# Kernel optimization log

Measured on AMD Instinct MI355X. Metric: run time of the kernel, lower is better.

Reference implementation:

```python
import jax, jax.numpy as jnp
import numpy as np

T, B, C, HF, H, W, E, TOP_K = 4, 32, 384, 1536, 14, 14, 8, 2
AUX_W = 0.01
ALPHA = 2.0  # spikingjelly ATan surrogate default

@jax.custom_vjp
def spike(v):
    return (v >= 0.0).astype(v.dtype)

def _spike_fwd(v):
    return spike(v), v

def _spike_bwd(v, g):
    sg = (ALPHA / 2.0) / (1.0 + (jnp.pi / 2.0 * ALPHA * v) ** 2)
    return (g * sg,)

spike.defvjp(_spike_fwd, _spike_bwd)

def lif_multistep(x, tau):
    # x: (T, ...). decay_input=True, v_threshold=1, hard reset to 0, detach_reset
    def step(v, xt):
        v = v + (xt - v) / tau
        s = spike(v - 1.0)
        v = v * (1.0 - jax.lax.stop_gradient(s))
        return v, s
    _, s = jax.lax.scan(step, jnp.zeros_like(x[0]), x)
    return s

def bn_eval(y, gamma, beta, mean, var, eps=1e-5):
    inv = gamma / jnp.sqrt(var + eps)
    return y * inv[None, :, None, None] + (beta - mean * inv)[None, :, None, None]

def setup_inputs() -> dict:
    key = jax.random.key(0)
    ks = jax.random.split(key, 8)
    d = {"x": jax.random.normal(ks[0], (T, B, C, H, W), jnp.float32)}
    d["rw"] = jax.random.normal(ks[1], (E, C), jnp.float32) * 0.02
    d["rb"] = jnp.zeros((E,), jnp.float32)
    d["r_gamma"] = jnp.ones((E,), jnp.float32)
    d["r_beta"] = jnp.zeros((E,), jnp.float32)
    d["r_mean"] = jax.random.normal(ks[2], (E,), jnp.float32) * 0.01
    d["r_var"] = jax.random.uniform(ks[3], (E,), jnp.float32, 0.75, 1.25)
    d["w1"] = jax.random.normal(ks[4], (E, HF, C), jnp.float32) * 0.02
    d["b1"] = jnp.zeros((E, HF), jnp.float32)
    d["g1"] = jnp.ones((E, HF), jnp.float32)
    d["be1"] = jnp.zeros((E, HF), jnp.float32)
    d["m1"] = jax.random.normal(ks[5], (E, HF), jnp.float32) * 0.01
    d["v1"] = jnp.ones((E, HF), jnp.float32)
    d["w2"] = jax.random.normal(ks[6], (E, C, HF), jnp.float32) * 0.02
    d["b2"] = jnp.zeros((E, C), jnp.float32)
    d["g2"] = jnp.ones((E, C), jnp.float32)
    d["be2"] = jnp.zeros((E, C), jnp.float32)
    d["m2"] = jax.random.normal(ks[7], (E, C), jnp.float32) * 0.01
    d["v2"] = jnp.ones((E, C), jnp.float32)
    d["taus"] = jnp.linspace(1.5, 4.0, E, dtype=jnp.float32)
    return d

def reference(x, rw, rb, r_gamma, r_beta, r_mean, r_var,
              w1, b1, g1, be1, m1, v1, w2, b2, g2, be2, m2, v2, taus):
    Tn, Bn, Cn, Hn, Wn = x.shape
    N = Tn * Bn
    # ---- SpikeRouter ----
    s = lif_multistep(x, 2.0)                                   # (T,B,C,H,W)
    r = jnp.einsum('tbchw,ec->tbehw', s, rw) + rb[None, None, :, None, None]
    r = bn_eval(r.reshape(N, E, Hn, Wn), r_gamma, r_beta, r_mean, r_var)
    logits = r.mean(axis=(-2, -1))                              # (N,E)
    probs = jax.nn.softmax(logits, axis=-1)
    tkw, tki = jax.lax.top_k(probs, TOP_K)
    tkw = tkw / tkw.sum(axis=-1, keepdims=True)
    one_hot = jax.nn.one_hot(tki, E, dtype=x.dtype)             # (N,K,E)
    gate = (one_hot * tkw[..., None]).sum(axis=1)               # (N,E), 0 for unselected
    # ---- expert dispatch/combine (dense, math-equivalent: gate==0 masks out) ----
    xt = x.reshape(N, Cn, Hn, Wn)
    out = jnp.zeros_like(xt)
    for e in range(E):
        s1 = spike(xt / taus[e] - 1.0)                          # T=1 LIF step
        h = jnp.einsum('nchw,oc->nohw', s1, w1[e]) + b1[e][None, :, None, None]
        h = bn_eval(h, g1[e], be1[e], m1[e], v1[e])
        s2 = spike(h / taus[e] - 1.0)
        o = jnp.einsum('nchw,oc->nohw', s2, w2[e]) + b2[e][None, :, None, None]
        o = bn_eval(o, g2[e], be2[e], m2[e], v2[e])
        o = o + xt                                              # final residual
        out = out + gate[:, e, None, None, None] * o
    # ---- Switch-style load balancing loss ----
    f = one_hot.sum(axis=1).mean(axis=0)                        # fraction routed per expert
    p = probs.mean(axis=0)
    aux = AUX_W * E * jnp.sum(f * p)
    return out.reshape(Tn, Bn, Cn, Hn, Wn), aux
```

## Files before the change

kernel.cpp:

```cpp
#include <hip/hip_runtime.h>
#include <hip/hip_bf16.h>
#include <cstdint>
#include <math.h>

#define T_  4
#define B_  32
#define C_  384
#define HF_ 1536
#define HW_ 196
#define E_  8
#define N_  128
#define NROW 1792
#define NGT  50176
#define LCAP 64

#define LIFW (B_ * C_ / 4)
#define TRB  (E_ * 12 * 24)
#define PRB  48
#define COMBB ((N_ * C_ * 49) / 256)

__global__ __launch_bounds__(256) void k_lifprep(
    const float* __restrict__ x, float* __restrict__ cnt,
    unsigned int* __restrict__ levels4,
    const float* __restrict__ w1, __hip_bfloat16* __restrict__ w1t,
    const float* b1, const float* g1, const float* be1,
    const float* m1, const float* v1,
    const float* b2, const float* g2, const float* be2,
    const float* m2, const float* v2,
    const float* taus,
    float* A, float* Bc, float* const2, float* inv2v,
    float* rowmaxp, int* header) {
  __shared__ float tile[64][33];
  int blk = blockIdx.x;
  int tid = threadIdx.x;

  if (blk < LIFW) {
    int lane = tid & 63, wave = tid >> 6;
    int bc = blk * 4 + wave;
    bool act = lane < 49;
    float te[E_];
    #pragma unroll
    for (int e2 = 0; e2 < E_; ++e2) {
      float t = taus[e2];
      float y = t;
      #pragma unroll
      for (int it = 0; it < 4; ++it) {
        float cnd = __uint_as_float(__float_as_uint(y) - 1u);
        if (cnd / t - 1.0f >= 0.0f) y = cnd; else break;
      }
      te[e2] = y;
    }
    const float4* xr = (const float4*)x;
    size_t rb = (size_t)bc * 49 + (act ? lane : 0);
    const size_t ts4 = (size_t)B_ * C_ * 49;
    float4 v = {0.f, 0.f, 0.f, 0.f};
    unsigned int counts = 0;
    unsigned int pk[T_];
    #pragma unroll
    for (int t = 0; t < T_; ++t) {
      float4 xv;
      if (act) xv = xr[rb + (size_t)t * ts4];
      else { xv.x = xv.y = xv.z = xv.w = -1e30f; }
      int l0 = 0, l1 = 0, l2 = 0, l3 = 0;
      #pragma unroll
      for (int e2 = 0; e2 < E_; ++e2) {
        l0 += (xv.x >= te[e2]) ? 1 : 0;
        l1 += (xv.y >= te[e2]) ? 1 : 0;
        l2 += (xv.z >= te[e2]) ? 1 : 0;
        l3 += (xv.w >= te[e2]) ? 1 : 0;
      }
      pk[t] = (unsigned int)l0 | ((unsigned int)l1 << 8) |
              ((unsigned int)l2 << 16) | ((unsigned int)l3 << 24);
      v.x = v.x + (xv.x - v.x) * 0.5f;
      v.y = v.y + (xv.y - v.y) * 0.5f;
      v.z = v.z + (xv.z - v.z) * 0.5f;
      v.w = v.w + (xv.w - v.w) * 0.5f;
      int cl = 0;
      if (v.x - 1.0f >= 0.0f) { v.x = 0.f; ++cl; }
      if (v.y - 1.0f >= 0.0f) { v.y = 0.f; ++cl; }
      if (v.z - 1.0f >= 0.0f) { v.z = 0.f; ++cl; }
      if (v.w - 1.0f >= 0.0f) { v.w = 0.f; ++cl; }
      counts += (unsigned int)cl << (8 * t);
    }
    if (act) {
      #pragma unroll
      for (int t = 0; t < T_; ++t)
        levels4[rb + (size_t)t * ts4] = pk[t];
    }
    #pragma unroll
    for (int off = 1; off < 64; off <<= 1)
      counts += (unsigned int)__shfl_xor((int)counts, off, 64);
    if (lane == 0) {
      #pragma unroll
      for (int t = 0; t < T_; ++t)
        cnt[(size_t)t * B_ * C_ + bc] = (float)((counts >> (8 * t)) & 0xffu);
    }
  } else if (blk < LIFW + TRB) {
    int rem = blk - LIFW;
    int e = rem / 288, r2 = rem % 288;
    int ct = r2 / 24, ot = r2 % 24;
    int c0 = ct * 32, o0 = ot * 64;
    int cl = tid & 31, olb = tid >> 5;
    #pragma unroll
    for (int it = 0; it < 8; ++it) {
      int ol = olb + it * 8;
      tile[ol][cl] = w1[(size_t)(e * HF_ + o0 + ol) * C_ + c0 + cl];
    }
    __syncthreads();
    int ol2 = tid & 63, clb = tid >> 6;
    #pragma unroll
    for (int it = 0; it < 8; ++it) {
      int cl2 = clb + it * 4;
      w1t[(size_t)(e * C_ + c0 + cl2) * HF_ + o0 + ol2] =
          __float2bfloat16(tile[ol2][cl2]);
    }
    if (tid < 32) {
      float m = 0.f;
      for (int ol = 0; ol < 64; ++ol) {
        float bv = __bfloat162float(__float2bfloat16(tile[ol][tid]));
        m = fmaxf(m, fabsf(bv));
      }
      rowmaxp[(size_t)(e * C_ + c0 + tid) * 24 + ot] = m;
    }
  } else {
    int idx = (blk - LIFW - TRB) * 256 + tid;
    if (idx < 64) header[idx] = 0;
    if (idx < E_ * HF_) {
      int e = idx / HF_;
      float inv = g1[idx] / sqrtf(v1[idx] + 1e-5f);
      float sh  = be1[idx] - m1[idx] * inv;
      A[idx]  = inv;
      Bc[idx] = inv * b1[idx] + sh - taus[e];
    }
    if (idx < E_ * C_) {
      float inv = g2[idx] / sqrtf(v2[idx] + 1e-5f);
      const2[idx] = b2[idx] * inv + (be2[idx] - m2[idx] * inv);
      inv2v[idx]  = inv;
    }
  }
}

__global__ __launch_bounds__(256) void k_router(
    const float* __restrict__ cnt, const float* __restrict__ rw,
    const float* rb, const float* rg, const float* rbeta,
    const float* rmean, const float* rvar,
    const float* __restrict__ const2,
    const float* __restrict__ rowmaxp, float* __restrict__ rowmax,
    const float* __restrict__ A, const float* __restrict__ Bc,
    float* __restrict__ thrmin,
    int* sel_e, float* sel_g, float* gsum, float* K,
    float* f_acc, float* p_acc) {
  __shared__ float sc[C_ + 256 + E_];
  __shared__ int s_i1, s_i2;
  __shared__ float s_g1, s_g2;
  int bid = blockIdx.x, tid = threadIdx.x;

  if (bid < N_) {
    int n = bid;
    float* part = sc + C_;
    float* lg = part + 256;
    for (int c = tid; c < C_; c += 256) sc[c] = cnt[(size_t)n * C_ + c];
    __syncthreads();
    {
      int e = tid >> 5, sub = tid & 31;
      float d = 0.f;
      for (int c = sub; c < C_; c += 32) d += rw[e * C_ + c] * sc[c];
      part[tid] = d;
    }
    __syncthreads();
    if (tid < E_) {
      float dot = 0.f;
      #pragma unroll
      for (int j = 0; j < 32; ++j) dot += part[tid * 32 + j];
      float inv = rg[tid] / sqrtf(rvar[tid] + 1e-5f);
      lg[tid] = (dot * (1.0f / HW_) + rb[tid]) * inv +
                (rbeta[tid] - rmean[tid] * inv);
    }
    __syncthreads();
    if (tid == 0) {
      float m = lg[0];
      for (int e = 1; e < E_; ++e) m = fmaxf(m, lg[e]);
      float pr[E_]; float s = 0.f;
      for (int e = 0; e < E_; ++e) { pr[e] = expf(lg[e] - m); s += pr[e]; }
      float invs = 1.0f / s;
      for (int e = 0; e < E_; ++e) pr[e] *= invs;
      int i1 = 0;
      for (int e = 1; e < E_; ++e) if (pr[e] > pr[i1]) i1 = e;
      int i2 = (i1 == 0) ? 1 : 0;
      for (int e = 0; e < E_; ++e) if (e != i1 && pr[e] > pr[i2]) i2 = e;
      float w = pr[i1] + pr[i2];
      float ga = pr[i1] / w, gb = pr[i2] / w;
      sel_e[2 * n] = i1; sel_e[2 * n + 1] = i2;
      sel_g[2 * n] = ga; sel_g[2 * n + 1] = gb;
      gsum[n] = ga + gb;
      s_i1 = i1; s_i2 = i2; s_g1 = ga; s_g2 = gb;
      atomicAdd(&f_acc[i1], 1.0f);
      atomicAdd(&f_acc[i2], 1.0f);
      for (int e = 0; e < E_; ++e) atomicAdd(&p_acc[e], pr[e]);
    }
    __syncthreads();
    int i1 = s_i1, i2 = s_i2; float ga = s_g1, gb = s_g2;
    for (int c = tid; c < C_; c += 256)
      K[(size_t)n * C_ + c] =
          ga * const2[i1 * C_ + c] + gb * const2[i2 * C_ + c];
  } else if (bid < N_ + 12) {
    int idx = (bid - N_) * 256 + tid;
    if (idx < E_ * C_) {
      float m = 0.f;
      #pragma unroll
      for (int t = 0; t < 24; ++t) m = fmaxf(m, rowmaxp[(size_t)idx * 24 + t]);
      rowmax[idx] = m;
    }
  } else {
    float* red = sc;
    for (int e = 0; e < E_; ++e) {
      float m = INFINITY;
      for (int o = tid; o < HF_; o += 256) {
        float a = A[e * HF_ + o], b = Bc[e * HF_ + o];
        float thr = (a != 0.0f) ? (-b / fabsf(a))
                                : ((b >= 0.0f) ? -INFINITY : INFINITY);
        m = fminf(m, thr);
      }
      red[tid] = m;
      __syncthreads();
      for (int s = 128; s > 0; s >>= 1) {
        if (tid < s) red[tid] = fminf(red[tid], red[tid + s]);
        __syncthreads();
      }
      if (tid == 0) thrmin[e] = red[0];
      __syncthreads();
    }
  }
}

__global__ __launch_bounds__(256) void k_lists(
    const float* __restrict__ x, const unsigned char* __restrict__ levels,
    const int* __restrict__ sel_e,
    const float* __restrict__ rowmax, const float* __restrict__ thrmin,
    unsigned short* __restrict__ list16,
    int* __restrict__ queue, int* __restrict__ qcount,
    const float* __restrict__ f_acc, const float* __restrict__ p_acc,
    float* __restrict__ aux_out,
    const float* __restrict__ gsum, const float* __restrict__ K,
    float* __restrict__ out) {
  __shared__ unsigned char xs8[14 * C_];
  int bid = blockIdx.x, tid = threadIdx.x;

  if (bid >= NROW) {
    int idx = (bid - NROW) * 256 + tid;
    int nc = idx / 49;
    float g = gsum[nc / C_];
    float kc = K[nc];
    float4 v = ((const float4*)x)[idx];
    v.x = g * v.x + kc;
    v.y = g * v.y + kc;
    v.z = g * v.z + kc;
    v.w = g * v.w + kc;
    ((float4*)out)[idx] = v;
    return;
  }

  int lane = tid & 63, wave = tid >> 6;
  int n = bid / 14, h = bid - n * 14;
  unsigned long long lmask = (1ull << lane) - 1ull;

  if (bid == 0 && tid == 0) {
    float s = 0.f;
    for (int e = 0; e < E_; ++e)
      s += (f_acc[e] * (1.0f / N_)) * (p_acc[e] * (1.0f / N_));
    *aux_out = 0.01f * E_ * s;
  }

  for (int c = tid; c < C_; c += 256) {
    const unsigned short* p =
        (const unsigned short*)(levels + (size_t)(n * C_ + c) * HW_ + h * 14);
    #pragma unroll
    for (int i = 0; i < 7; ++i) {
      unsigned short u = p[i];
      xs8[(2 * i) * C_ + c]     = (unsigned char)(u & 0xff);
      xs8[(2 * i + 1) * C_ + c] = (unsigned char)(u >> 8);
    }
  }
  __syncthreads();

  for (int t = wave; t < 28; t += 4) {
    int k = t / 14, w = t - k * 14;
    int pair = 2 * n + k;
    int e = sel_e[pair];
    const float* rme = rowmax + e * C_;
    unsigned long long masks[6];
    int nnz = 0;
    float myb = 0.f;
    #pragma unroll
    for (int cb = 0; cb < 6; ++cb) {
      int c = cb * 64 + lane;
      bool sp = ((int)xs8[w * C_ + c] > e);
      unsigned long long m = __ballot(sp);
      masks[cb] = m;
      if (sp) myb += rme[c];
      nnz += __popcll(m);
    }
    #pragma unroll
    for (int off = 1; off < 64; off <<= 1) myb += __shfl_xor(myb, off, 64);
    bool prune = (myb < thrmin[e] - 1e-4f);
    if (!prune) {
      int tw = pair * 196 + h * 14 + w;
      size_t lbase = (size_t)tw * LCAP;
      int cum = 0;
      #pragma unroll
      for (int cb = 0; cb < 6; ++cb) {
        unsigned long long m = masks[cb];
        bool sp = (m >> lane) & 1ull;
        int pos = cum + __popcll(m & lmask);
        if (sp && pos < LCAP) list16[lbase + pos] = (unsigned short)(cb * 64 + lane);
        cum += __popcll(m);
      }
      if (lane == 0) {
        int nv = nnz < LCAP ? nnz : LCAP;
        int qi = atomicAdd(qcount, 1);
        queue[qi] = tw | (nv << 20);
      }
    }
  }
}

__global__ __launch_bounds__(256, 4) void k_gather(
    const __hip_bfloat16* __restrict__ w1t,
    const float* __restrict__ A, const float* __restrict__ Bc,
    const int* __restrict__ sel_e, const float* __restrict__ sel_g,
    const int* __restrict__ queue, const int* __restrict__ qcount,
    const unsigned short* __restrict__ list16,
    const float* __restrict__ inv2v, const float* __restrict__ w2,
    float* __restrict__ out) {
  int nq = *qcount;
  int wid = blockIdx.x * 4 + (threadIdx.x >> 6);
  int lane = threadIdx.x & 63;
  int nwaves = gridDim.x * 4;

  for (int qi = wid; qi < nq; qi += nwaves) {
    int ent = queue[qi];
    int tw = ent & 0xFFFFF;
    int nnz = ent >> 20;
    int pair = tw / HW_, pos = tw - pair * HW_;
    int n = pair >> 1;
    int e = sel_e[pair];
    int lv = (int)list16[(size_t)tw * LCAP + lane];
    const uint4* wb = (const uint4*)(w1t + (size_t)e * C_ * HF_);

    #pragma unroll
    for (int pass = 0; pass < 3; ++pass) {
      const uint4* wbp = wb + pass * 64 + lane;
      float acc[8];
      #pragma unroll
      for (int q = 0; q < 8; ++q) acc[q] = 0.f;
      int j = 0;
      for (; j + 4 <= nnz; j += 4) {
        int c0 = __shfl(lv, j + 0);
        int c1 = __shfl(lv, j + 1);
        int c2 = __shfl(lv, j + 2);
        int c3 = __shfl(lv, j + 3);
        uint4 a = wbp[c0 * 192];
        uint4 b = wbp[c1 * 192];
        uint4 c = wbp[c2 * 192];
        uint4 d = wbp[c3 * 192];
        uint32_t ua[4] = {a.x, a.y, a.z, a.w};
        uint32_t ub[4] = {b.x, b.y, b.z, b.w};
        uint32_t uc[4] = {c.x, c.y, c.z, c.w};
        uint32_t ud[4] = {d.x, d.y, d.z, d.w};
        #pragma unroll
        for (int q = 0; q < 4; ++q) {
          acc[2 * q]     += __uint_as_float(ua[q] << 16) + __uint_as_float(ub[q] << 16) +
                            __uint_as_float(uc[q] << 16) + __uint_as_float(ud[q] << 16);
          acc[2 * q + 1] += __uint_as_float(ua[q] & 0xffff0000u) + __uint_as_float(ub[q] & 0xffff0000u) +
                            __uint_as_float(uc[q] & 0xffff0000u) + __uint_as_float(ud[q] & 0xffff0000u);
        }
      }
      for (; j < nnz; ++j) {
        int c0 = __shfl(lv, j);
        uint4 a = wbp[c0 * 192];
        uint32_t ua[4] = {a.x, a.y, a.z, a.w};
        #pragma unroll
        for (int q = 0; q < 4; ++q) {
          acc[2 * q]     += __uint_as_float(ua[q] << 16);
          acc[2 * q + 1] += __uint_as_float(ua[q] & 0xffff0000u);
        }
      }
      int k2 = (pass * 64 + lane) * 2;
      float4 Av0 = ((const float4*)(A + e * HF_))[k2];
      float4 Av1 = ((const float4*)(A + e * HF_))[k2 + 1];
      float4 Bv0 = ((const float4*)(Bc + e * HF_))[k2];
      float4 Bv1 = ((const float4*)(Bc + e * HF_))[k2 + 1];
      float av[8] = {Av0.x, Av0.y, Av0.z, Av0.w, Av1.x, Av1.y, Av1.z, Av1.w};
      float bv[8] = {Bv0.x, Bv0.y, Bv0.z, Bv0.w, Bv1.x, Bv1.y, Bv1.z, Bv1.w};
      #pragma unroll
      for (int q = 0; q < 8; ++q) {
        unsigned long long fm = __ballot(av[q] * acc[q] + bv[q] >= 0.0f);
        while (fm) {
          int b = __ffsll((unsigned long long)fm) - 1;
          fm &= fm - 1;
          int o = (pass * 64 + b) * 8 + q;
          float gk = sel_g[pair];
          const float* w2r = w2 + (size_t)e * C_ * HF_ + o;
          const float* ivr = inv2v + e * C_;
          for (int c = lane; c < C_; c += 64) {
            atomicAdd(&out[((size_t)(n * C_ + c)) * HW_ + pos],
                      gk * ivr[c] * w2r[(size_t)c * HF_]);
          }
        }
      }
    }
  }
}

extern "C" void kernel_launch(void* const* d_in, const int* in_sizes, int n_in,
                              void* d_out, int out_size, void* d_ws, size_t ws_size,
                              hipStream_t stream) {
  const float* x       = (const float*)d_in[0];
  const float* rw      = (const float*)d_in[1];
  const float* rb      = (const float*)d_in[2];
  const float* r_gamma = (const float*)d_in[3];
  const float* r_beta  = (const float*)d_in[4];
  const float* r_mean  = (const float*)d_in[5];
  const float* r_var   = (const float*)d_in[6];
  const float* w1      = (const float*)d_in[7];
  const float* b1      = (const float*)d_in[8];
  const float* g1      = (const float*)d_in[9];
  const float* be1     = (const float*)d_in[10];
  const float* m1      = (const float*)d_in[11];
  const float* v1      = (const float*)d_in[12];
  const float* w2      = (const float*)d_in[13];
  const float* b2      = (const float*)d_in[14];
  const float* g2      = (const float*)d_in[15];
  const float* be2     = (const float*)d_in[16];
  const float* m2      = (const float*)d_in[17];
  const float* v2      = (const float*)d_in[18];
  const float* taus    = (const float*)d_in[19];
  float* out = (float*)d_out;

  char* ws = (char*)d_ws;
  int*   header = (int*)ws;
  float* f_acc  = (float*)ws + 8;
  float* p_acc  = (float*)ws + 16;
  float* cnt    = (float*)(ws + 256);
  int*   sel_e  = (int*)(ws + 196864);
  float* sel_g  = (float*)(ws + 197888);
  float* gsum   = (float*)(ws + 198912);
  float* K      = (float*)(ws + 199424);
  float* A      = (float*)(ws + 396032);
  float* Bc     = (float*)(ws + 445184);
  float* const2 = (float*)(ws + 494336);
  float* inv2v  = (float*)(ws + 506624);
  __hip_bfloat16* w1t = (__hip_bfloat16*)(ws + 715520);
  int*   queue  = (int*)(ws + 10152704);
  unsigned short* list16 = (unsigned short*)(ws + 10353408);
  float* rowmaxp = (float*)(ws + 16775936);
  float* rowmax  = (float*)(ws + 17070848);
  float* thrmin  = (float*)(ws + 17083136);
  unsigned char* levels = (unsigned char*)(ws + 17084416);
  int* qcount = header + 1;

  k_lifprep<<<LIFW + TRB + PRB, 256, 0, stream>>>(
      x, cnt, (unsigned int*)levels, w1, w1t,
      b1, g1, be1, m1, v1, b2, g2, be2, m2, v2, taus,
      A, Bc, const2, inv2v, rowmaxp, header);
  k_router<<<N_ + 13, 256, 0, stream>>>(
      cnt, rw, rb, r_gamma, r_beta, r_mean, r_var, const2,
      rowmaxp, rowmax, A, Bc, thrmin,
      sel_e, sel_g, gsum, K, f_acc, p_acc);
  k_lists<<<NROW + COMBB, 256, 0, stream>>>(
      x, levels, sel_e, rowmax, thrmin, list16, queue, qcount,
      f_acc, p_acc, out + (out_size - 1), gsum, K, out);
  k_gather<<<2048, 256, 0, stream>>>(
      w1t, A, Bc, sel_e, sel_g, queue, qcount, list16, inv2v, w2, out);
}
```

Before: 201.4 us.

## Fuse four kernel stages into one cooperative persistent kernel with grid syncs

Replaces the four separate launches (LIF/prep, router, list building, gather) with a single cooperative kernel. Each stage runs as a grid-stride loop over the old block indices, and grid.sync() separates the stages. The aim is to remove per-launch overhead and the gaps between kernels. In exchange, each stage is limited to a grid sized by occupancy (at most 1024 blocks), grid-wide barriers are added, and the grid size is cached in a static variable.

```diff
diff --git a/kernel.cpp b/kernel.cpp
--- a/kernel.cpp
+++ b/kernel.cpp
@@ -1,7 +1,10 @@
 #include <hip/hip_runtime.h>
 #include <hip/hip_bf16.h>
+#include <hip/hip_cooperative_groups.h>
 #include <cstdint>
 #include <math.h>
+
+namespace cg = cooperative_groups;
 
 #define T_  4
 #define B_  32
@@ -19,457 +22,451 @@
 #define PRB  48
 #define COMBB ((N_ * C_ * 49) / 256)
 
-__global__ __launch_bounds__(256) void k_lifprep(
-    const float* __restrict__ x, float* __restrict__ cnt,
-    unsigned int* __restrict__ levels4,
-    const float* __restrict__ w1, __hip_bfloat16* __restrict__ w1t,
-    const float* b1, const float* g1, const float* be1,
-    const float* m1, const float* v1,
-    const float* b2, const float* g2, const float* be2,
-    const float* m2, const float* v2,
-    const float* taus,
-    float* A, float* Bc, float* const2, float* inv2v,
-    float* rowmaxp, int* header) {
-  __shared__ float tile[64][33];
-  int blk = blockIdx.x;
+struct FP {
+  const float *x, *rw, *rbv, *rg, *rbeta, *rmean, *rvar, *w1;
+  const float *b1, *g1, *be1, *m1, *v1;
+  const float *w2, *b2, *g2, *be2, *m2, *v2, *taus;
+  float *out, *aux;
+  int *header;
+  float *f_acc, *p_acc;
+  float *cnt;
+  int *sel_e; float *sel_g, *gsum, *K;
+  float *A, *Bc, *const2, *inv2v;
+  __hip_bfloat16 *w1t;
+  int *queue;
+  unsigned short *list16;
+  float *rowmaxp, *rowmax, *thrmin;
+  unsigned char *levels;
+};
+
+__global__ __launch_bounds__(256, 4) void k_fused(FP p) {
+  __shared__ __align__(16) char smraw[8448];
+  __shared__ int s_i1, s_i2;
+  __shared__ float s_g1, s_g2;
+  cg::grid_group grid = cg::this_grid();
   int tid = threadIdx.x;
-
-  if (blk < LIFW) {
-    int lane = tid & 63, wave = tid >> 6;
-    int bc = blk * 4 + wave;
-    bool act = lane < 49;
-    float te[E_];
-    #pragma unroll
-    for (int e2 = 0; e2 < E_; ++e2) {
-      float t = taus[e2];
-      float y = t;
-      #pragma unroll
-      for (int it = 0; it < 4; ++it) {
-        float cnd = __uint_as_float(__float_as_uint(y) - 1u);
-        if (cnd / t - 1.0f >= 0.0f) y = cnd; else break;
-      }
-      te[e2] = y;
+  int gsz = gridDim.x;
+
+  for (int blk = blockIdx.x; blk < LIFW + TRB + PRB; blk += gsz) {
+    if (blk < LIFW) {
+      int lane = tid & 63, wave = tid >> 6;
+      int bc = blk * 4 + wave;
+      bool act = lane < 49;
+      float te[E_];
+      #pragma unroll
+      for (int e2 = 0; e2 < E_; ++e2) {
+        float t = p.taus[e2];
+        float y = t;
+        #pragma unroll
+        for (int it = 0; it < 4; ++it) {
+          float cnd = __uint_as_float(__float_as_uint(y) - 1u);
+          if (cnd / t - 1.0f >= 0.0f) y = cnd; else break;
+        }
+        te[e2] = y;
+      }
+      const float4* xr = (const float4*)p.x;
+      unsigned int* levels4 = (unsigned int*)p.levels;
+      size_t rowb = (size_t)bc * 49 + (act ? lane : 0);
+      const size_t ts4 = (size_t)B_ * C_ * 49;
+      float4 v = {0.f, 0.f, 0.f, 0.f};
+      unsigned int counts = 0;
+      unsigned int pk[T_];
+      #pragma unroll
+      for (int t = 0; t < T_; ++t) {
+        float4 xv;
+        if (act) xv = xr[rowb + (size_t)t * ts4];
+        else { xv.x = xv.y = xv.z = xv.w = -1e30f; }
+        int l0 = 0, l1 = 0, l2 = 0, l3 = 0;
+        #pragma unroll
+        for (int e2 = 0; e2 < E_; ++e2) {
+          l0 += (xv.x >= te[e2]) ? 1 : 0;
+          l1 += (xv.y >= te[e2]) ? 1 : 0;
+          l2 += (xv.z >= te[e2]) ? 1 : 0;
+          l3 += (xv.w >= te[e2]) ? 1 : 0;
+        }
+        pk[t] = (unsigned int)l0 | ((unsigned int)l1 << 8) |
+                ((unsigned int)l2 << 16) | ((unsigned int)l3 << 24);
+        v.x = v.x + (xv.x - v.x) * 0.5f;
+        v.y = v.y + (xv.y - v.y) * 0.5f;
+        v.z = v.z + (xv.z - v.z) * 0.5f;
+        v.w = v.w + (xv.w - v.w) * 0.5f;
+        int cl = 0;
+        if (v.x - 1.0f >= 0.0f) { v.x = 0.f; ++cl; }
+        if (v.y - 1.0f >= 0.0f) { v.y = 0.f; ++cl; }
+        if (v.z - 1.0f >= 0.0f) { v.z = 0.f; ++cl; }
+        if (v.w - 1.0f >= 0.0f) { v.w = 0.f; ++cl; }
+        counts += (unsigned int)cl << (8 * t);
+      }
+      if (act) {
+        #pragma unroll
+        for (int t = 0; t < T_; ++t)
+          levels4[rowb + (size_t)t * ts4] = pk[t];
+      }
+      #pragma unroll
+      for (int off = 1; off < 64; off <<= 1)
+        counts += (unsigned int)__shfl_xor((int)counts, off, 64);
+      if (lane == 0) {
+        #pragma unroll
+        for (int t = 0; t < T_; ++t)
+          p.cnt[(size_t)t * B_ * C_ + bc] = (float)((counts >> (8 * t)) & 0xffu);
+      }
+    } else if (blk < LIFW + TRB) {
+      float (*tile)[33] = (float(*)[33])smraw;
+      __syncthreads();
+      int rem = blk - LIFW;
+      int e = rem / 288, r2 = rem % 288;
+      int ct = r2 / 24, ot = r2 % 24;
+      int c0 = ct * 32, o0 = ot * 64;
+      int cl = tid & 31, olb = tid >> 5;
+      #pragma unroll
+      for (int it = 0; it < 8; ++it) {
+        int ol = olb + it * 8;
+        tile[ol][cl] = p.w1[(size_t)(e * HF_ + o0 + ol) * C_ + c0 + cl];
+      }
+      __syncthreads();
+      int ol2 = tid & 63, clb = tid >> 6;
+      #pragma unroll
+      for (int it = 0; it < 8; ++it) {
+        int cl2 = clb + it * 4;
+        p.w1t[(size_t)(e * C_ + c0 + cl2) * HF_ + o0 + ol2] =
+            __float2bfloat16(tile[ol2][cl2]);
+      }
+      if (tid < 32) {
+        float m = 0.f;
+        for (int ol = 0; ol < 64; ++ol) {
+          float bv = __bfloat162float(__float2bfloat16(tile[ol][tid]));
+          m = fmaxf(m, fabsf(bv));
+        }
+        p.rowmaxp[(size_t)(e * C_ + c0 + tid) * 24 + ot] = m;
+      }
+    } else {
+      int idx = (blk - LIFW - TRB) * 256 + tid;
+      if (idx < 64) p.header[idx] = 0;
+      if (idx < E_ * HF_) {
+        int e = idx / HF_;
+        float inv = p.g1[idx] / sqrtf(p.v1[idx] + 1e-5f);
+        float sh  = p.be1[idx] - p.m1[idx] * inv;
+        p.A[idx]  = inv;
+        p.Bc[idx] = inv * p.b1[idx] + sh - p.taus[e];
+      }
+      if (idx < E_ * C_) {
+        float inv = p.g2[idx] / sqrtf(p.v2[idx] + 1e-5f);
+        p.const2[idx] = p.b2[idx] * inv + (p.be2[idx] - p.m2[idx] * inv);
+        p.inv2v[idx]  = inv;
+      }
     }
-    const float4* xr = (const float4*)x;
-    size_t rb = (size_t)bc * 49 + (act ? lane : 0);
-    const size_t ts4 = (size_t)B_ * C_ * 49;
-    float4 v = {0.f, 0.f, 0.f, 0.f};
-    unsigned int counts = 0;
-    unsigned int pk[T_];
-    #pragma unroll
-    for (int t = 0; t < T_; ++t) {
-      float4 xv;
-      if (act) xv = xr[rb + (size_t)t * ts4];
-      else { xv.x = xv.y = xv.z = xv.w = -1e30f; }
-      int l0 = 0, l1 = 0, l2 = 0, l3 = 0;
-      #pragma unroll
-      for (int e2 = 0; e2 < E_; ++e2) {
-        l0 += (xv.x >= te[e2]) ? 1 : 0;
-        l1 += (xv.y >= te[e2]) ? 1 : 0;
-        l2 += (xv.z >= te[e2]) ? 1 : 0;
-        l3 += (xv.w >= te[e2]) ? 1 : 0;
-      }
-      pk[t] = (unsigned int)l0 | ((unsigned int)l1 << 8) |
-              ((unsigned int)l2 << 16) | ((unsigned int)l3 << 24);
-      v.x = v.x + (xv.x - v.x) * 0.5f;
-      v.y = v.y + (xv.y - v.y) * 0.5f;
-      v.z = v.z + (xv.z - v.z) * 0.5f;
-      v.w = v.w + (xv.w - v.w) * 0.5f;
-      int cl = 0;
-      if (v.x - 1.0f >= 0.0f) { v.x = 0.f; ++cl; }
-      if (v.y - 1.0f >= 0.0f) { v.y = 0.f; ++cl; }
-      if (v.z - 1.0f >= 0.0f) { v.z = 0.f; ++cl; }
-      if (v.w - 1.0f >= 0.0f) { v.w = 0.f; ++cl; }
-      counts += (unsigned int)cl << (8 * t);
+  }
+  grid.sync();
+
+  for (int bid = blockIdx.x; bid < N_ + 13; bid += gsz) {
+    float* sc = (float*)smraw;
+    if (bid < N_) {
+      int n = bid;
+      float* part = sc + C_;
+      float* lg = part + 256;
+      for (int c = tid; c < C_; c += 256) sc[c] = p.cnt[(size_t)n * C_ + c];
+      __syncthreads();
+      {
+        int e = tid >> 5, sub = tid & 31;
+        float d = 0.f;
+        for (int c = sub; c < C_; c += 32) d += p.rw[e * C_ + c] * sc[c];
+        part[tid] = d;
+      }
+      __syncthreads();
+      if (tid < E_) {
+        float dot = 0.f;
+        #pragma unroll
+        for (int j = 0; j < 32; ++j) dot += part[tid * 32 + j];
+        float inv = p.rg[tid] / sqrtf(p.rvar[tid] + 1e-5f);
+        lg[tid] = (dot * (1.0f / HW_) + p.rbv[tid]) * inv +
+                  (p.rbeta[tid] - p.rmean[tid] * inv);
+      }
+      __syncthreads();
+      if (tid == 0) {
+        float m = lg[0];
+        for (int e = 1; e < E_; ++e) m = fmaxf(m, lg[e]);
+        float pr[E_]; float s = 0.f;
+        for (int e = 0; e < E_; ++e) { pr[e] = expf(lg[e] - m); s += pr[e]; }
+        float invs = 1.0f / s;
+        for (int e = 0; e < E_; ++e) pr[e] *= invs;
+        int i1 = 0;
+        for (int e = 1; e < E_; ++e) if (pr[e] > pr[i1]) i1 = e;
+        int i2 = (i1 == 0) ? 1 : 0;
+        for (int e = 0; e < E_; ++e) if (e != i1 && pr[e] > pr[i2]) i2 = e;
+        float w = pr[i1] + pr[i2];
+        float ga = pr[i1] / w, gb = pr[i2] / w;
+        p.sel_e[2 * n] = i1; p.sel_e[2 * n + 1] = i2;
+        p.sel_g[2 * n] = ga; p.sel_g[2 * n + 1] = gb;
+        p.gsum[n] = ga + gb;
+        s_i1 = i1; s_i2 = i2; s_g1 = ga; s_g2 = gb;
+        atomicAdd(&p.f_acc[i1], 1.0f);
+        atomicAdd(&p.f_acc[i2], 1.0f);
+        for (int e = 0; e < E_; ++e) atomicAdd(&p.p_acc[e], pr[e]);
+      }
+      __syncthreads();
+      int i1 = s_i1, i2 = s_i2; float ga = s_g1, gb = s_g2;
+      for (int c = tid; c < C_; c += 256)
+        p.K[(size_t)n * C_ + c] =
+            ga * p.const2[i1 * C_ + c] + gb * p.const2[i2 * C_ + c];
+    } else if (bid < N_ + 12) {
+      int idx = (bid - N_) * 256 + tid;
+      if (idx < E_ * C_) {
+        float m = 0.f;
+        #pragma unroll
+        for (int t = 0; t < 24; ++t)
+          m = fmaxf(m, p.rowmaxp[(size_t)idx * 24 + t]);
+        p.rowmax[idx] = m;
+      }
+    } else {
+      float* red = sc;
+      for (int e = 0; e < E_; ++e) {
+        float m = INFINITY;
+        for (int o = tid; o < HF_; o += 256) {
+          float a = p.A[e * HF_ + o], b = p.Bc[e * HF_ + o];
+          float thr = (a != 0.0f) ? (-b / fabsf(a))
+                                  : ((b >= 0.0f) ? -INFINITY : INFINITY);
+          m = fminf(m, thr);
+        }
+        red[tid] = m;
+        __syncthreads();
+        for (int s = 128; s > 0; s >>= 1) {
+          if (tid < s) red[tid] = fminf(red[tid], red[tid + s]);
+          __syncthreads();
+        }
+        if (tid == 0) p.thrmin[e] = red[0];
+        __syncthreads();
+      }
     }
-    if (act) {
-      #pragma unroll
-      for (int t = 0; t < T_; ++t)
-        levels4[rb + (size_t)t * ts4] = pk[t];
+  }
+  grid.sync();
+
+  for (int bid = blockIdx.x; bid < NROW + COMBB; bid += gsz) {
+    if (bid >= NROW) {
+      int idx = (bid - NROW) * 256 + tid;
+      int nc = idx / 49;
+      float g = p.gsum[nc / C_];
+      float kc = p.K[nc];
+      float4 v = ((const float4*)p.x)[idx];
+      v.x = g * v.x + kc;
+      v.y = g * v.y + kc;
+      v.z = g * v.z + kc;
+      v.w = g * v.w + kc;
+      ((float4*)p.out)[idx] = v;
+    } else {
+      unsigned char* xs8 = (unsigned char*)smraw;
+      __syncthreads();
+      int lane = tid & 63, wave = tid >> 6;
+      int n = bid / 14, h = bid - n * 14;
+      unsigned long long lmask = (1ull << lane) - 1ull;
+
+      if (bid == 0 && tid == 0) {
+        float s = 0.f;
+        for (int e = 0; e < E_; ++e)
+          s += (p.f_acc[e] * (1.0f / N_)) * (p.p_acc[e] * (1.0f / N_));
+        *p.aux = 0.01f * E_ * s;
+      }
+
+      for (int c = tid; c < C_; c += 256) {
+        const unsigned short* pp =
+            (const unsigned short*)(p.levels + (size_t)(n * C_ + c) * HW_ + h * 14);
+        #pragma unroll
+        for (int i = 0; i < 7; ++i) {
+          unsigned short u = pp[i];
+          xs8[(2 * i) * C_ + c]     = (unsigned char)(u & 0xff);
+          xs8[(2 * i + 1) * C_ + c] = (unsigned char)(u >> 8);
+        }
+      }
+      __syncthreads();
+
+      for (int t = wave; t < 28; t += 4) {
+        int k = t / 14, w = t - k * 14;
+        int pair = 2 * n + k;
+        int e = p.sel_e[pair];
+        const float* rme = p.rowmax + e * C_;
+        unsigned long long masks[6];
+        int nnz = 0;
+        float myb = 0.f;
+        #pragma unroll
+        for (int cb = 0; cb < 6; ++cb) {
+          int c = cb * 64 + lane;
+          bool sp = ((int)xs8[w * C_ + c] > e);
+          unsigned long long m = __ballot(sp);
+          masks[cb] = m;
+          if (sp) myb += rme[c];
+          nnz += __popcll(m);
+        }
+        #pragma unroll
+        for (int off = 1; off < 64; off <<= 1) myb += __shfl_xor(myb, off, 64);
+        bool prune = (myb < p.thrmin[e] - 1e-4f);
+        if (!prune) {
+          int tw = pair * 196 + h * 14 + w;
+          size_t lbase = (size_t)tw * LCAP;
+          int cum = 0;
+          #pragma unroll
+          for (int cb = 0; cb < 6; ++cb) {
+            unsigned long long m = masks[cb];
+            bool sp = (m >> lane) & 1ull;
+            int pos = cum + __popcll(m & lmask);
+            if (sp && pos < LCAP)
+              p.list16[lbase + pos] = (unsigned short)(cb * 64 + lane);
+            cum += __popcll(m);
+          }
+          if (lane == 0) {
+            int nv = nnz < LCAP ? nnz : LCAP;
+            int qi = atomicAdd(&p.header[1], 1);
+            p.queue[qi] = tw | (nv << 20);
+          }
+        }
+      }
     }
-    #pragma unroll
-    for (int off = 1; off < 64; off <<= 1)
-      counts += (unsigned int)__shfl_xor((int)counts, off, 64);
-    if (lane == 0) {
-      #pragma unroll
-      for (int t = 0; t < T_; ++t)
-        cnt[(size_t)t * B_ * C_ + bc] = (float)((counts >> (8 * t)) & 0xffu);
-    }
-  } else if (blk < LIFW + TRB) {
-    int rem = blk - LIFW;
-    int e = rem / 288, r2 = rem % 288;
-    int ct = r2 / 24, ot = r2 % 24;
-    int c0 = ct * 32, o0 = ot * 64;
-    int cl = tid & 31, olb = tid >> 5;
-    #pragma unroll
-    for (int it = 0; it < 8; ++it) {
-      int ol = olb + it * 8;
-      tile[ol][cl] = w1[(size_t)(e * HF_ + o0 + ol) * C_ + c0 + cl];
-    }
-    __syncthreads();
-    int ol2 = tid & 63, clb = tid >> 6;
-    #pragma unroll
-    for (int it = 0; it < 8; ++it) {
-      int cl2 = clb + it * 4;
-      w1t[(size_t)(e * C_ + c0 + cl2) * HF_ + o0 + ol2] =
-          __float2bfloat16(tile[ol2][cl2]);
-    }
-    if (tid < 32) {
-      float m = 0.f;
-      for (int ol = 0; ol < 64; ++ol) {
-        float bv = __bfloat162float(__float2bfloat16(tile[ol][tid]));
-        m = fmaxf(m, fabsf(bv));
-      }
-      rowmaxp[(size_t)(e * C_ + c0 + tid) * 24 + ot] = m;
-    }
-  } else {
-    int idx = (blk - LIFW - TRB) * 256 + tid;
-    if (idx < 64) header[idx] = 0;
-    if (idx < E_ * HF_) {
-      int e = idx / HF_;
-      float inv = g1[idx] / sqrtf(v1[idx] + 1e-5f);
-      float sh  = be1[idx] - m1[idx] * inv;
-      A[idx]  = inv;
-      Bc[idx] = inv * b1[idx] + sh - taus[e];
-    }
-    if (idx < E_ * C_) {
-      float inv = g2[idx] / sqrtf(v2[idx] + 1e-5f);
-      const2[idx] = b2[idx] * inv + (be2[idx] - m2[idx] * inv);
-      inv2v[idx]  = inv;
+  }
+  grid.sync();
+
+  {
+    int nq = p.header[1];
+    int wid = blockIdx.x * 4 + (tid >> 6);
+    int lane = tid & 63;
+    int nwaves = gsz * 4;
+
+    for (int qi = wid; qi < nq; qi += nwaves) {
+      int ent = p.queue[qi];
+      int tw = ent & 0xFFFFF;
+      int nnz = ent >> 20;
+      int pair = tw / HW_, pos = tw - pair * HW_;
+      int n = pair >> 1;
+      int e = p.sel_e[pair];
+      int lv = (int)p.list16[(size_t)tw * LCAP + lane];
+      const uint4* wb = (const uint4*)(p.w1t + (size_t)e * C_ * HF_);
+
+      #pragma unroll
+      for (int pass = 0; pass < 3; ++pass) {
+        const uint4* wbp = wb + pass * 64 + lane;
+        float acc[8];
+        #pragma unroll
+        for (int q = 0; q < 8; ++q) acc[q] = 0.f;
+        int j = 0;
+        for (; j + 4 <= nnz; j += 4) {
+          int c0 = __shfl(lv, j + 0);
+          int c1 = __shfl(lv, j + 1);
+          int c2 = __shfl(lv, j + 2);
+          int c3 = __shfl(lv, j + 3);
+          uint4 a = wbp[c0 * 192];
+          uint4 b = wbp[c1 * 192];
+          uint4 c = wbp[c2 * 192];
+          uint4 d = wbp[c3 * 192];
+          uint32_t ua[4] = {a.x, a.y, a.z, a.w};
+          uint32_t ub[4] = {b.x, b.y, b.z, b.w};
+          uint32_t uc[4] = {c.x, c.y, c.z, c.w};
+          uint32_t ud[4] = {d.x, d.y, d.z, d.w};
+          #pragma unroll
+          for (int q = 0; q < 4; ++q) {
+            acc[2 * q]     += __uint_as_float(ua[q] << 16) + __uint_as_float(ub[q] << 16) +
+                              __uint_as_float(uc[q] << 16) + __uint_as_float(ud[q] << 16);
+            acc[2 * q + 1] += __uint_as_float(ua[q] & 0xffff0000u) + __uint_as_float(ub[q] & 0xffff0000u) +
+                              __uint_as_float(uc[q] & 0xffff0000u) + __uint_as_float(ud[q] & 0xffff0000u);
+          }
+        }
+        for (; j < nnz; ++j) {
+          int c0 = __shfl(lv, j);
+          uint4 a = wbp[c0 * 192];
+          uint32_t ua[4] = {a.x, a.y, a.z, a.w};
+          #pragma unroll
+          for (int q = 0; q < 4; ++q) {
+            acc[2 * q]     += __uint_as_float(ua[q] << 16);
+            acc[2 * q + 1] += __uint_as_float(ua[q] & 0xffff0000u);
+          }
+        }
+        int k2 = (pass * 64 + lane) * 2;
+        float4 Av0 = ((const float4*)(p.A + e * HF_))[k2];
+        float4 Av1 = ((const float4*)(p.A + e * HF_))[k2 + 1];
+        float4 Bv0 = ((const float4*)(p.Bc + e * HF_))[k2];
+        float4 Bv1 = ((const float4*)(p.Bc + e * HF_))[k2 + 1];
+        float av[8] = {Av0.x, Av0.y, Av0.z, Av0.w, Av1.x, Av1.y, Av1.z, Av1.w};
+        float bv[8] = {Bv0.x, Bv0.y, Bv0.z, Bv0.w, Bv1.x, Bv1.y, Bv1.z, Bv1.w};
+        #pragma unroll
+        for (int q = 0; q < 8; ++q) {
+          unsigned long long fm = __ballot(av[q] * acc[q] + bv[q] >= 0.0f);
+          while (fm) {
+            int b = __ffsll(fm) - 1;
+            fm &= fm - 1;
+            int o = (pass * 64 + b) * 8 + q;
+            float gk = p.sel_g[pair];
+            const float* w2r = p.w2 + (size_t)e * C_ * HF_ + o;
+            const float* ivr = p.inv2v + e * C_;
+            for (int c = lane; c < C_; c += 64) {
+              atomicAdd(&p.out[((size_t)(n * C_ + c)) * HW_ + pos],
+                        gk * ivr[c] * w2r[(size_t)c * HF_]);
+            }
+          }
+        }
+      }
     }
   }
 }
 
-__global__ __launch_bounds__(256) void k_router(
-    const float* __restrict__ cnt, const float* __restrict__ rw,
-    const float* rb, const float* rg, const float* rbeta,
-    const float* rmean, const float* rvar,
-    const float* __restrict__ const2,
-    const float* __restrict__ rowmaxp, float* __restrict__ rowmax,
-    const float* __restrict__ A, const float* __restrict__ Bc,
-    float* __restrict__ thrmin,
-    int* sel_e, float* sel_g, float* gsum, float* K,
-    float* f_acc, float* p_acc) {
-  __shared__ float sc[C_ + 256 + E_];
-  __shared__ int s_i1, s_i2;
-  __shared__ float s_g1, s_g2;
-  int bid = blockIdx.x, tid = threadIdx.x;
-
-  if (bid < N_) {
-    int n = bid;
-    float* part = sc + C_;
-    float* lg = part + 256;
-    for (int c = tid; c < C_; c += 256) sc[c] = cnt[(size_t)n * C_ + c];
-    __syncthreads();
-    {
-      int e = tid >> 5, sub = tid & 31;
-      float d = 0.f;
-      for (int c = sub; c < C_; c += 32) d += rw[e * C_ + c] * sc[c];
-      part[tid] = d;
-    }
-    __syncthreads();
-    if (tid < E_) {
-      float dot = 0.f;
-      #pragma unroll
-      for (int j = 0; j < 32; ++j) dot += part[tid * 32 + j];
-      float inv = rg[tid] / sqrtf(rvar[tid] + 1e-5f);
-      lg[tid] = (dot * (1.0f / HW_) + rb[tid]) * inv +
-                (rbeta[tid] - rmean[tid] * inv);
-    }
-    __syncthreads();
-    if (tid == 0) {
-      float m = lg[0];
-      for (int e = 1; e < E_; ++e) m = fmaxf(m, lg[e]);
-      float pr[E_]; float s = 0.f;
-      for (int e = 0; e < E_; ++e) { pr[e] = expf(lg[e] - m); s += pr[e]; }
-      float invs = 1.0f / s;
-      for (int e = 0; e < E_; ++e) pr[e] *= invs;
-      int i1 = 0;
-      for (int e = 1; e < E_; ++e) if (pr[e] > pr[i1]) i1 = e;
-      int i2 = (i1 == 0) ? 1 : 0;
-      for (int e = 0; e < E_; ++e) if (e != i1 && pr[e] > pr[i2]) i2 = e;
-      float w = pr[i1] + pr[i2];
-      float ga = pr[i1] / w, gb = pr[i2] / w;
-      sel_e[2 * n] = i1; sel_e[2 * n + 1] = i2;
-      sel_g[2 * n] = ga; sel_g[2 * n + 1] = gb;
-      gsum[n] = ga + gb;
-      s_i1 = i1; s_i2 = i2; s_g1 = ga; s_g2 = gb;
-      atomicAdd(&f_acc[i1], 1.0f);
-      atomicAdd(&f_acc[i2], 1.0f);
-      for (int e = 0; e < E_; ++e) atomicAdd(&p_acc[e], pr[e]);
-    }
-    __syncthreads();
-    int i1 = s_i1, i2 = s_i2; float ga = s_g1, gb = s_g2;
-    for (int c = tid; c < C_; c += 256)
-      K[(size_t)n * C_ + c] =
-          ga * const2[i1 * C_ + c] + gb * const2[i2 * C_ + c];
-  } else if (bid < N_ + 12) {
-    int idx = (bid - N_) * 256 + tid;
-    if (idx < E_ * C_) {
-      float m = 0.f;
-      #pragma unroll
-      for (int t = 0; t < 24; ++t) m = fmaxf(m, rowmaxp[(size_t)idx * 24 + t]);
-      rowmax[idx] = m;
-    }
-  } else {
-    float* red = sc;
-    for (int e = 0; e < E_; ++e) {
-      float m = INFINITY;
-      for (int o = tid; o < HF_; o += 256) {
-        float a = A[e * HF_ + o], b = Bc[e * HF_ + o];
-        float thr = (a != 0.0f) ? (-b / fabsf(a))
-                                : ((b >= 0.0f) ? -INFINITY : INFINITY);
-        m = fminf(m, thr);
-      }
-      red[tid] = m;
-      __syncthreads();
-      for (int s = 128; s > 0; s >>= 1) {
-        if (tid < s) red[tid] = fminf(red[tid], red[tid + s]);
-        __syncthreads();
-      }
-      if (tid == 0) thrmin[e] = red[0];
-      __syncthreads();
-    }
-  }
-}
-
-__global__ __launch_bounds__(256) void k_lists(
-    const float* __restrict__ x, const unsigned char* __restrict__ levels,
-    const int* __restrict__ sel_e,
-    const float* __restrict__ rowmax, const float* __restrict__ thrmin,
-    unsigned short* __restrict__ list16,
-    int* __restrict__ queue, int* __restrict__ qcount,
-    const float* __restrict__ f_acc, const float* __restrict__ p_acc,
-    float* __restrict__ aux_out,
-    const float* __restrict__ gsum, const float* __restrict__ K,
-    float* __restrict__ out) {
-  __shared__ unsigned char xs8[14 * C_];
-  int bid = blockIdx.x, tid = threadIdx.x;
-
-  if (bid >= NROW) {
-    int idx = (bid - NROW) * 256 + tid;
-    int nc = idx / 49;
-    float g = gsum[nc / C_];
-    float kc = K[nc];
-    float4 v = ((const float4*)x)[idx];
-    v.x = g * v.x + kc;
-    v.y = g * v.y + kc;
-    v.z = g * v.z + kc;
-    v.w = g * v.w + kc;
-    ((float4*)out)[idx] = v;
-    return;
-  }
-
-  int lane = tid & 63, wave = tid >> 6;
-  int n = bid / 14, h = bid - n * 14;
-  unsigned long long lmask = (1ull << lane) - 1ull;
-
-  if (bid == 0 && tid == 0) {
-    float s = 0.f;
-    for (int e = 0; e < E_; ++e)
-      s += (f_acc[e] * (1.0f / N_)) * (p_acc[e] * (1.0f / N_));
-    *aux_out = 0.01f * E_ * s;
-  }
-
-  for (int c = tid; c < C_; c += 256) {
-    const unsigned short* p =
-        (const unsigned short*)(levels + (size_t)(n * C_ + c) * HW_ + h * 14);
-    #pragma unroll
-    for (int i = 0; i < 7; ++i) {
-      unsigned short u = p[i];
-      xs8[(2 * i) * C_ + c]     = (unsigned char)(u & 0xff);
-      xs8[(2 * i + 1) * C_ + c] = (unsigned char)(u >> 8);
-    }
-  }
-  __syncthreads();
-
-  for (int t = wave; t < 28; t += 4) {
-    int k = t / 14, w = t - k * 14;
-    int pair = 2 * n + k;
-    int e = sel_e[pair];
-    const float* rme = rowmax + e * C_;
-    unsigned long long masks[6];
-    int nnz = 0;
-    float myb = 0.f;
-    #pragma unroll
-    for (int cb = 0; cb < 6; ++cb) {
-      int c = cb * 64 + lane;
-      bool sp = ((int)xs8[w * C_ + c] > e);
-      unsigned long long m = __ballot(sp);
-      masks[cb] = m;
-      if (sp) myb += rme[c];
-      nnz += __popcll(m);
-    }
-    #pragma unroll
-    for (int off = 1; off < 64; off <<= 1) myb += __shfl_xor(myb, off, 64);
-    bool prune = (myb < thrmin[e] - 1e-4f);
-    if (!prune) {
-      int tw = pair * 196 + h * 14 + w;
-      size_t lbase = (size_t)tw * LCAP;
-      int cum = 0;
-      #pragma unroll
-      for (int cb = 0; cb < 6; ++cb) {
-        unsigned long long m = masks[cb];
-        bool sp = (m >> lane) & 1ull;
-        int pos = cum + __popcll(m & lmask);
-        if (sp && pos < LCAP) list16[lbase + pos] = (unsigned short)(cb * 64 + lane);
-        cum += __popcll(m);
-      }
-      if (lane == 0) {
-        int nv = nnz < LCAP ? nnz : LCAP;
-        int qi = atomicAdd(qcount, 1);
-        queue[qi] = tw | (nv << 20);
-      }
-    }
-  }
-}
-
-__global__ __launch_bounds__(256, 4) void k_gather(
-    const __hip_bfloat16* __restrict__ w1t,
-    const float* __restrict__ A, const float* __restrict__ Bc,
-    const int* __restrict__ sel_e, const float* __restrict__ sel_g,
-    const int* __restrict__ queue, const int* __restrict__ qcount,
-    const unsigned short* __restrict__ list16,
-    const float* __restrict__ inv2v, const float* __restrict__ w2,
-    float* __restrict__ out) {
-  int nq = *qcount;
-  int wid = blockIdx.x * 4 + (threadIdx.x >> 6);
-  int lane = threadIdx.x & 63;
-  int nwaves = gridDim.x * 4;
-
-  for (int qi = wid; qi < nq; qi += nwaves) {
-    int ent = queue[qi];
-    int tw = ent & 0xFFFFF;
-    int nnz = ent >> 20;
-    int pair = tw / HW_, pos = tw - pair * HW_;
-    int n = pair >> 1;
-    int e = sel_e[pair];
-    int lv = (int)list16[(size_t)tw * LCAP + lane];
-    const uint4* wb = (const uint4*)(w1t + (size_t)e * C_ * HF_);
-
-    #pragma unroll
-    for (int pass = 0; pass < 3; ++pass) {
-      const uint4* wbp = wb + pass * 64 + lane;
-      float acc[8];
-      #pragma unroll
-      for (int q = 0; q < 8; ++q) acc[q] = 0.f;
-      int j = 0;
-      for (; j + 4 <= nnz; j += 4) {
-        int c0 = __shfl(lv, j + 0);
-        int c1 = __shfl(lv, j + 1);
-        int c2 = __shfl(lv, j + 2);
-        int c3 = __shfl(lv, j + 3);
-        uint4 a = wbp[c0 * 192];
-        uint4 b = wbp[c1 * 192];
-        uint4 c = wbp[c2 * 192];
-        uint4 d = wbp[c3 * 192];
-        uint32_t ua[4] = {a.x, a.y, a.z, a.w};
-        uint32_t ub[4] = {b.x, b.y, b.z, b.w};
-        uint32_t uc[4] = {c.x, c.y, c.z, c.w};
-        uint32_t ud[4] = {d.x, d.y, d.z, d.w};
-        #pragma unroll
-        for (int q = 0; q < 4; ++q) {
-          acc[2 * q]     += __uint_as_float(ua[q] << 16) + __uint_as_float(ub[q] << 16) +
-                            __uint_as_float(uc[q] << 16) + __uint_as_float(ud[q] << 16);
-          acc[2 * q + 1] += __uint_as_float(ua[q] & 0xffff0000u) + __uint_as_float(ub[q] & 0xffff0000u) +
-                            __uint_as_float(uc[q] & 0xffff0000u) + __uint_as_float(ud[q] & 0xffff0000u);
-        }
-      }
-      for (; j < nnz; ++j) {
-        int c0 = __shfl(lv, j);
-        uint4 a = wbp[c0 * 192];
-        uint32_t ua[4] = {a.x, a.y, a.z, a.w};
-        #pragma unroll
-        for (int q = 0; q < 4; ++q) {
-          acc[2 * q]     += __uint_as_float(ua[q] << 16);
-          acc[2 * q + 1] += __uint_as_float(ua[q] & 0xffff0000u);
-        }
-      }
-      int k2 = (pass * 64 + lane) * 2;
-      float4 Av0 = ((const float4*)(A + e * HF_))[k2];
-      float4 Av1 = ((const float4*)(A + e * HF_))[k2 + 1];
-      float4 Bv0 = ((const float4*)(Bc + e * HF_))[k2];
-      float4 Bv1 = ((const float4*)(Bc + e * HF_))[k2 + 1];
-      float av[8] = {Av0.x, Av0.y, Av0.z, Av0.w, Av1.x, Av1.y, Av1.z, Av1.w};
-      float bv[8] = {Bv0.x, Bv0.y, Bv0.z, Bv0.w, Bv1.x, Bv1.y, Bv1.z, Bv1.w};
-      #pragma unroll
-      for (int q = 0; q < 8; ++q) {
-        unsigned long long fm = __ballot(av[q] * acc[q] + bv[q] >= 0.0f);
-        while (fm) {
-          int b = __ffsll((unsigned long long)fm) - 1;
-          fm &= fm - 1;
-          int o = (pass * 64 + b) * 8 + q;
-          float gk = sel_g[pair];
-          const float* w2r = w2 + (size_t)e * C_ * HF_ + o;
-          const float* ivr = inv2v + e * C_;
-          for (int c = lane; c < C_; c += 64) {
-            atomicAdd(&out[((size_t)(n * C_ + c)) * HW_ + pos],
-                      gk * ivr[c] * w2r[(size_t)c * HF_]);
-          }
-        }
-      }
-    }
-  }
-}
-
 extern "C" void kernel_launch(void* const* d_in, const int* in_sizes, int n_in,
                               void* d_out, int out_size, void* d_ws, size_t ws_size,
                               hipStream_t stream) {
-  const float* x       = (const float*)d_in[0];
-  const float* rw      = (const float*)d_in[1];
-  const float* rb      = (const float*)d_in[2];
-  const float* r_gamma = (const float*)d_in[3];
-  const float* r_beta  = (const float*)d_in[4];
-  const float* r_mean  = (const float*)d_in[5];
-  const float* r_var   = (const float*)d_in[6];
-  const float* w1      = (const float*)d_in[7];
-  const float* b1      = (const float*)d_in[8];
-  const float* g1      = (const float*)d_in[9];
-  const float* be1     = (const float*)d_in[10];
-  const float* m1      = (const float*)d_in[11];
-  const float* v1      = (const float*)d_in[12];
-  const float* w2      = (const float*)d_in[13];
-  const float* b2      = (const float*)d_in[14];
-  const float* g2      = (const float*)d_in[15];
-  const float* be2     = (const float*)d_in[16];
-  const float* m2      = (const float*)d_in[17];
-  const float* v2      = (const float*)d_in[18];
-  const float* taus    = (const float*)d_in[19];
-  float* out = (float*)d_out;
-
   char* ws = (char*)d_ws;
-  int*   header = (int*)ws;
-  float* f_acc  = (float*)ws + 8;
-  float* p_acc  = (float*)ws + 16;
-  float* cnt    = (float*)(ws + 256);
-  int*   sel_e  = (int*)(ws + 196864);
-  float* sel_g  = (float*)(ws + 197888);
-  float* gsum   = (float*)(ws + 198912);
-  float* K      = (float*)(ws + 199424);
-  float* A      = (float*)(ws + 396032);
-  float* Bc     = (float*)(ws + 445184);
-  float* const2 = (float*)(ws + 494336);
-  float* inv2v  = (float*)(ws + 506624);
-  __hip_bfloat16* w1t = (__hip_bfloat16*)(ws + 715520);
-  int*   queue  = (int*)(ws + 10152704);
-  unsigned short* list16 = (unsigned short*)(ws + 10353408);
-  float* rowmaxp = (float*)(ws + 16775936);
-  float* rowmax  = (float*)(ws + 17070848);
-  float* thrmin  = (float*)(ws + 17083136);
-  unsigned char* levels = (unsigned char*)(ws + 17084416);
-  int* qcount = header + 1;
-
-  k_lifprep<<<LIFW + TRB + PRB, 256, 0, stream>>>(
-      x, cnt, (unsigned int*)levels, w1, w1t,
-      b1, g1, be1, m1, v1, b2, g2, be2, m2, v2, taus,
-      A, Bc, const2, inv2v, rowmaxp, header);
-  k_router<<<N_ + 13, 256, 0, stream>>>(
-      cnt, rw, rb, r_gamma, r_beta, r_mean, r_var, const2,
-      rowmaxp, rowmax, A, Bc, thrmin,
-      sel_e, sel_g, gsum, K, f_acc, p_acc);
-  k_lists<<<NROW + COMBB, 256, 0, stream>>>(
-      x, levels, sel_e, rowmax, thrmin, list16, queue, qcount,
-      f_acc, p_acc, out + (out_size - 1), gsum, K, out);
-  k_gather<<<2048, 256, 0, stream>>>(
-      w1t, A, Bc, sel_e, sel_g, queue, qcount, list16, inv2v, w2, out);
+  FP p;
+  p.x      = (const float*)d_in[0];
+  p.rw     = (const float*)d_in[1];
+  p.rbv    = (const float*)d_in[2];
+  p.rg     = (const float*)d_in[3];
+  p.rbeta  = (const float*)d_in[4];
+  p.rmean  = (const float*)d_in[5];
+  p.rvar   = (const float*)d_in[6];
+  p.w1     = (const float*)d_in[7];
+  p.b1     = (const float*)d_in[8];
+  p.g1     = (const float*)d_in[9];
+  p.be1    = (const float*)d_in[10];
+  p.m1     = (const float*)d_in[11];
+  p.v1     = (const float*)d_in[12];
+  p.w2     = (const float*)d_in[13];
+  p.b2     = (const float*)d_in[14];
+  p.g2     = (const float*)d_in[15];
+  p.be2    = (const float*)d_in[16];
+  p.m2     = (const float*)d_in[17];
+  p.v2     = (const float*)d_in[18];
+  p.taus   = (const float*)d_in[19];
+  p.out    = (float*)d_out;
+  p.aux    = (float*)d_out + (out_size - 1);
+  p.header = (int*)ws;
+  p.f_acc  = (float*)ws + 8;
+  p.p_acc  = (float*)ws + 16;
+  p.cnt    = (float*)(ws + 256);
+  p.sel_e  = (int*)(ws + 196864);
+  p.sel_g  = (float*)(ws + 197888);
+  p.gsum   = (float*)(ws + 198912);
+  p.K      = (float*)(ws + 199424);
+  p.A      = (float*)(ws + 396032);
+  p.Bc     = (float*)(ws + 445184);
+  p.const2 = (float*)(ws + 494336);
+  p.inv2v  = (float*)(ws + 506624);
+  p.w1t    = (__hip_bfloat16*)(ws + 715520);
+  p.queue  = (int*)(ws + 10152704);
+  p.list16 = (unsigned short*)(ws + 10353408);
+  p.rowmaxp= (float*)(ws + 16775936);
+  p.rowmax = (float*)(ws + 17070848);
+  p.thrmin = (float*)(ws + 17083136);
+  p.levels = (unsigned char*)(ws + 17084416);
+
+  static int s_grid = 0;
+  if (s_grid == 0) {
+    int nb = 0;
+    hipOccupancyMaxActiveBlocksPerMultiprocessor(&nb, (const void*)k_fused, 256, 0);
+    if (nb < 1) nb = 1;
+    int dev = 0;
+    hipGetDevice(&dev);
+    hipDeviceProp_t prop;
+    hipGetDeviceProperties(&prop, dev);
+    int g = nb * prop.multiProcessorCount;
+    if (g > 1024) g = 1024;
+    if (g < 256) g = 256;
+    s_grid = g;
+  }
+
+  void* args[] = {&p};
+  hipLaunchCooperativeKernel((const void*)k_fused, dim3(s_grid), dim3(256),
+                             args, 0, stream);
 }
```

After: 449.5 us. 123% more time.
